# Performance work log

Measured on AMD Instinct MI355X. Metric: run time of the kernel, lower is better.

Reference implementation:

```python
import jax, jax.numpy as jnp
import numpy as np

SMOOTH = 1.0
P = 2
NUM_ITERS = 200  # kornia connected_components num_iterations


def _maxpool3x3(x):
    # F.max_pool2d(x, kernel_size=3, stride=1, padding=1) equivalent (NCHW)
    return jax.lax.reduce_window(
        x, -jnp.inf, jax.lax.max,
        window_dimensions=(1, 1, 3, 3),
        window_strides=(1, 1, 1, 1),
        padding='SAME',
    )


def connected_components(mask_f, num_iterations=NUM_ITERS):
    # kornia-style iterative label propagation on a (B,1,H,W) binary mask.
    # labels initialized to unique pixel ids where mask==1, 0 elsewhere,
    # then 3x3 max-pool propagated, keeping background pinned at 0.
    B, C, H, W = mask_f.shape
    mask = mask_f > 0
    init = jnp.arange(B * C * H * W, dtype=mask_f.dtype).reshape(B, C, H, W)
    out = jnp.where(mask, init, 0.0)

    def body(i, o):
        return jnp.where(mask, _maxpool3x3(o), 0.0)

    return jax.lax.fori_loop(0, num_iterations, body, out)


def setup_inputs() -> dict:
    key = jax.random.key(0)
    k1, k2 = jax.random.split(key)
    B, H, W = 16, 512, 512
    predict = jax.random.uniform(k1, (B, 1, H, W), dtype=jnp.float32)
    target = jax.random.uniform(k2, (B, 1, H, W), dtype=jnp.float32)
    return {"predict": predict, "target": target}


def reference(predict, target):
    B = predict.shape[0]
    # threshold at half of global max -> binary mask (non-differentiable)
    binmask = (predict > (predict.max() / 2)).astype(predict.dtype)
    labels = connected_components(jax.lax.stop_gradient(binmask))

    # torch.numel(torch.unique(labels)) via sort + adjacent-diff count (jit-safe)
    s = jnp.sort(labels.reshape(-1))
    n_unique = 1 + jnp.sum(s[1:] != s[:-1])

    penalty = n_unique.astype(jnp.float32) / B
    penalty = jnp.where(penalty < 1.0, jnp.float32(B), penalty)
    penalty = jnp.minimum(penalty, jnp.float32(B))

    p = predict.reshape(B, -1)
    t = target.reshape(B, -1)
    num = jnp.sum(p * t, axis=1) + SMOOTH
    den = jnp.sum(p ** P + t ** P, axis=1) + SMOOTH
    loss = 1.0 - num / den
    return loss.mean() * penalty  # reduction='mean'
```

## Files before the change

kernel.cpp:

```cpp
#include <hip/hip_runtime.h>
#include <hip/hip_cooperative_groups.h>
#include <stdint.h>

namespace cg = cooperative_groups;

#define NPIX   (16 * 512 * 512)
#define IMG    (512 * 512)
#define NB     16

#define CORE   64
#define HALO   8
#define KIT    8
#define NROUND 25
#define TILE   80
#define TW     88
#define TH     82
#define TX0    4

#define BM_WORDS  (NPIX / 32)
#define NREP      16
#define SAT       256u
#define MAX3(a, b, c) max(max((a), (b)), (c))

__global__ __launch_bounds__(256) void k_max(const float4* __restrict__ p, unsigned int* umax) {
    unsigned int m = 0;
    int base = blockIdx.x * 1024;
#pragma unroll
    for (int k = 0; k < 4; ++k) {
        float4 v = p[base + k * 256 + threadIdx.x];
        m = max(m, __float_as_uint(v.x));
        m = max(m, __float_as_uint(v.y));
        m = max(m, __float_as_uint(v.z));
        m = max(m, __float_as_uint(v.w));
    }
    for (int o = 32; o > 0; o >>= 1)
        m = max(m, (unsigned int)__shfl_down(m, o, 64));
    __shared__ unsigned int sm[4];
    int lane = threadIdx.x & 63, w = threadIdx.x >> 6;
    if (lane == 0) sm[w] = m;
    __syncthreads();
    if (threadIdx.x == 0)
        atomicMax(umax, max(max(sm[0], sm[1]), max(sm[2], sm[3])));
}

__global__ __launch_bounds__(256) void k_init(const float4* __restrict__ pr4,
                                              const float4* __restrict__ tg4,
                                              const unsigned int* __restrict__ umax,
                                              int4* __restrict__ lab4,
                                              float* __restrict__ num, float* __restrict__ den) {
    const float thr = __uint_as_float(*umax) * 0.5f;
    float sn = 0.f, sd = 0.f;
    int base = blockIdx.x * 1024;
#pragma unroll
    for (int k = 0; k < 4; ++k) {
        int i4 = base + k * 256 + threadIdx.x;
        float4 p = pr4[i4], t = tg4[i4];
        int pix = i4 * 4;
        int4 L;
        L.x = (p.x > thr) ? pix     : -1;
        L.y = (p.y > thr) ? pix + 1 : -1;
        L.z = (p.z > thr) ? pix + 2 : -1;
        L.w = (p.w > thr) ? pix + 3 : -1;
        lab4[i4] = L;
        sn += p.x * t.x + p.y * t.y + p.z * t.z + p.w * t.w;
        sd += p.x * p.x + p.y * p.y + p.z * p.z + p.w * p.w
            + t.x * t.x + t.y * t.y + t.z * t.z + t.w * t.w;
    }
    for (int o = 32; o > 0; o >>= 1) {
        sn += __shfl_down(sn, o, 64);
        sd += __shfl_down(sd, o, 64);
    }
    __shared__ float wn[4], wd[4];
    int lane = threadIdx.x & 63, w = threadIdx.x >> 6;
    if (lane == 0) { wn[w] = sn; wd[w] = sd; }
    __syncthreads();
    if (threadIdx.x == 0) {
        int b = blockIdx.x >> 6;
        atomicAdd(&num[b * 32], wn[0] + wn[1] + wn[2] + wn[3]);
        atomicAdd(&den[b * 32], wd[0] + wd[1] + wd[2] + wd[3]);
    }
}

__global__ __launch_bounds__(256) void k_iso(const int* __restrict__ lab,
                                             unsigned int* __restrict__ isoCnt) {
    unsigned int cnt = 0;
    const int tid = threadIdx.x;
    for (int k = 0; k < 8; ++k) {
        int i4 = (blockIdx.x * 8 + k) * 256 + tid;
        int px = i4 * 4;
        int y = (px >> 9) & 511;
        int gxr = px & 511;
        int4 c = *(const int4*)(lab + px);
        int lc = (gxr > 0)   ? lab[px - 1] : -1;
        int rc = (gxr < 508) ? lab[px + 4] : -1;
        int4 u; int lu, ru;
        if (y > 0) {
            u  = *(const int4*)(lab + px - 512);
            lu = (gxr > 0)   ? lab[px - 513] : -1;
            ru = (gxr < 508) ? lab[px - 508] : -1;
        } else { u = make_int4(-1, -1, -1, -1); lu = -1; ru = -1; }
        int4 d; int ld, rd;
        if (y < 511) {
            d  = *(const int4*)(lab + px + 512);
            ld = (gxr > 0)   ? lab[px + 511] : -1;
            rd = (gxr < 508) ? lab[px + 516] : -1;
        } else { d = make_int4(-1, -1, -1, -1); ld = -1; rd = -1; }
        int v0 = max(u.x, d.x), v1 = max(u.y, d.y), v2 = max(u.z, d.z), v3 = max(u.w, d.w);
        int cmL = MAX3(lu, lc, ld), cmR = MAX3(ru, rc, rd);
        int cm0 = max(v0, c.x), cm1 = max(v1, c.y), cm2 = max(v2, c.z), cm3 = max(v3, c.w);
        int nb0 = MAX3(cmL, cm1, v0);
        int nb1 = MAX3(cm0, cm2, v1);
        int nb2 = MAX3(cm1, cm3, v2);
        int nb3 = MAX3(cm2, cmR, v3);
        cnt += (c.x >= 0 && nb0 < 0 && px > 0) ? 1u : 0u;
        cnt += (c.y >= 0 && nb1 < 0) ? 1u : 0u;
        cnt += (c.z >= 0 && nb2 < 0) ? 1u : 0u;
        cnt += (c.w >= 0 && nb3 < 0) ? 1u : 0u;
    }
    for (int o = 32; o > 0; o >>= 1)
        cnt += __shfl_down(cnt, o, 64);
    __shared__ unsigned int sc[4];
    int lane = tid & 63, w = tid >> 6;
    if (lane == 0) sc[w] = cnt;
    __syncthreads();
    if (tid == 0)
        atomicAdd(isoCnt, sc[0] + sc[1] + sc[2] + sc[3]);
}

__global__ __launch_bounds__(256, 4) void k_prop_all(int* __restrict__ bufA,
                                                     int* __restrict__ bufB,
                                                     const unsigned int* __restrict__ isoCnt) {
    if (*isoCnt >= SAT) return;
    cg::grid_group grid = cg::this_grid();
    __shared__ int T[TH * TW];
    const int tid  = threadIdx.x;
    const int blk  = blockIdx.x;
    const int bx   = blk & 7, by = (blk >> 3) & 7, bimg = blk >> 6;
    const int gx0  = bx * CORE - HALO;
    const int gy0  = by * CORE - HALO;
    int* const base0 = bufA + bimg * IMG;
    int* const base1 = bufB + bimg * IMG;

    if (tid < TW) { T[tid] = -1; T[81 * TW + tid] = -1; }
    if (tid < 80) { T[(tid + 1) * TW + 3] = -1; T[(tid + 1) * TW + 84] = -1; }
    for (int u = tid; u < 1600; u += 256) {
        int r = u / 20, c = (u % 20) * 4;
        int gy = gy0 + r, gx = gx0 + c;
        int4 v = (gy >= 0 && gy < 512 && gx >= 0 && gx < 512)
                 ? *(const int4*)(base0 + (gy << 9) + gx)
                 : make_int4(-1, -1, -1, -1);
        *(int4*)&T[(r + 1) * TW + TX0 + c] = v;
    }
    __syncthreads();
    grid.sync();

    const bool active = (tid < 200);
    const int cu = tid % 20, ru = tid / 20;
    const int x0 = cu * 4;
    const int yr = ru * 8;
    int4 O[8];

#define LOAD_ROW(y, V, VL, VR) do {                            \
        const int* _r = &T[((y) + 1) * TW + TX0 + x0];         \
        V  = *(const int4*)_r;                                 \
        VL = _r[-1];                                           \
        VR = _r[4];                                            \
    } while (0)

    for (int r = 0; r < NROUND; ++r) {
        for (int it = 0; it < KIT; ++it) {
            if (active) {
                int4 A, B, C; int Al, Ar, Bl, Br, Cl, Cr;
                LOAD_ROW(yr - 1, A, Al, Ar);
                LOAD_ROW(yr,     B, Bl, Br);
#pragma unroll
                for (int j = 0; j < 8; ++j) {
                    LOAD_ROW(yr + j + 1, C, Cl, Cr);
                    int4 col;
                    col.x = MAX3(A.x, B.x, C.x);
                    col.y = MAX3(A.y, B.y, C.y);
                    col.z = MAX3(A.z, B.z, C.z);
                    col.w = MAX3(A.w, B.w, C.w);
                    int cl = MAX3(Al, Bl, Cl);
                    int cr = MAX3(Ar, Br, Cr);
                    O[j].x = MAX3(cl,    col.x, col.y) | (B.x >> 31);
                    O[j].y = MAX3(col.x, col.y, col.z) | (B.y >> 31);
                    O[j].z = MAX3(col.y, col.z, col.w) | (B.z >> 31);
                    O[j].w = MAX3(col.z, col.w, cr)    | (B.w >> 31);
                    A = B; Al = Bl; Ar = Br;
                    B = C; Bl = Cl; Br = Cr;
                }
            }
            __syncthreads();
            if (active) {
#pragma unroll
                for (int j = 0; j < 8; ++j)
                    *(int4*)&T[(yr + j + 1) * TW + TX0 + x0] = O[j];
            }
            __syncthreads();
        }

        if (r < NROUND - 1) {
            int* dst = (r & 1) ? base1 : base0;
            for (int u = tid; u < 448; u += 256) {
                int lr, lc;
                if (u < 128)      { lr = u >> 4;                lc = u & 15; }
                else if (u < 256) { lr = 56 + ((u - 128) >> 4); lc = u & 15; }
                else { int v = u - 256; lr = 8 + (v >> 2); int s = v & 3; lc = (s < 2) ? s : 12 + s; }
                int4 val = *(const int4*)&T[(HALO + lr + 1) * TW + TX0 + HALO + lc * 4];
                *(int4*)(dst + ((by * CORE + lr) << 9) + bx * CORE + lc * 4) = val;
            }
            __threadfence();
            grid.sync();
            const int* src = (r & 1) ? base1 : base0;
            for (int u = tid; u < 576; u += 256) {
                int lrow, lcu;
                if (u < 160)      { lrow = u / 20;              lcu = u % 20; }
                else if (u < 320) { lrow = 72 + (u - 160) / 20; lcu = u % 20; }
                else { int v = u - 320; lrow = 8 + (v >> 2); int s = v & 3; lcu = (s < 2) ? s : 16 + s; }
                int gy = gy0 + lrow, gx = gx0 + lcu * 4;
                int4 val = (gy >= 0 && gy < 512 && gx >= 0 && gx < 512)
                           ? *(const int4*)(src + (gy << 9) + gx)
                           : make_int4(-1, -1, -1, -1);
                *(int4*)&T[(lrow + 1) * TW + TX0 + lcu * 4] = val;
            }
            __syncthreads();
        } else {
            for (int u = tid; u < 1024; u += 256) {
                int lr = u >> 4, lc = u & 15;
                int4 val = *(const int4*)&T[(HALO + lr + 1) * TW + TX0 + HALO + lc * 4];
                *(int4*)(base0 + ((by * CORE + lr) << 9) + bx * CORE + lc * 4) = val;
            }
        }
    }
#undef LOAD_ROW
}

__global__ __launch_bounds__(256) void k_bits(const int* __restrict__ lab,
                                              unsigned int* __restrict__ bm,
                                              const unsigned int* __restrict__ isoCnt) {
    if (*isoCnt >= SAT) return;
    __shared__ unsigned int sk[1024];
    __shared__ int slot[256];
    const int tid = threadIdx.x;
    unsigned int* rep = bm + (blockIdx.x & (NREP - 1)) * BM_WORDS;
    for (int k = 0; k < 4; ++k) {
        if (k) __syncthreads();
        const int i4 = blockIdx.x * 1024 + k * 256 + tid;
        int4 c = ((const int4*)lab)[i4];
        int pw = __shfl_up(c.w, 1, 64);
        unsigned int prevk;
        if ((tid & 63) == 0) {
            if (i4 == 0) prevk = ~0u;
            else { int pv = lab[i4 * 4 - 1]; prevk = (pv < 0) ? 0u : (unsigned int)pv; }
        } else {
            prevk = (pw < 0) ? 0u : (unsigned int)pw;
        }
        unsigned int k0 = (c.x < 0) ? 0u : (unsigned int)c.x;
        unsigned int k1 = (c.y < 0) ? 0u : (unsigned int)c.y;
        unsigned int k2 = (c.z < 0) ? 0u : (unsigned int)c.z;
        unsigned int k3 = (c.w < 0) ? 0u : (unsigned int)c.w;
        bool c0 = (k0 != prevk), c1 = (k1 != k0), c2 = (k2 != k1), c3 = (k3 != k2);
        sk[0 * 256 + tid] = k0;
        sk[1 * 256 + tid] = k1;
        sk[2 * 256 + tid] = k2;
        sk[3 * 256 + tid] = k3;
        if (c0) slot[k0 & 255] = tid * 4 + 0;
        if (c1) slot[k1 & 255] = tid * 4 + 1;
        if (c2) slot[k2 & 255] = tid * 4 + 2;
        if (c3) slot[k3 & 255] = tid * 4 + 3;
        __syncthreads();
#define SKAT(w) sk[((w) & 3) * 256 + ((w) >> 2)]
        if (c0) { int w = slot[k0 & 255]; if (w != tid * 4 + 0 && SKAT(w) == k0) c0 = false; }
        if (c1) { int w = slot[k1 & 255]; if (w != tid * 4 + 1 && SKAT(w) == k1) c1 = false; }
        if (c2) { int w = slot[k2 & 255]; if (w != tid * 4 + 2 && SKAT(w) == k2) c2 = false; }
        if (c3) { int w = slot[k3 & 255]; if (w != tid * 4 + 3 && SKAT(w) == k3) c3 = false; }
#undef SKAT
#define TSET(kk, cc) if (cc) {                                        \
            unsigned int word = rep[(kk) >> 5];                       \
            if (!((word >> ((kk) & 31)) & 1u))                        \
                atomicOr(&rep[(kk) >> 5], 1u << ((kk) & 31));         \
        }
        TSET(k0, c0); TSET(k1, c1); TSET(k2, c2); TSET(k3, c3);
#undef TSET
    }
}

__global__ void k_popc(const unsigned int* __restrict__ bm, unsigned int* nuniq, int words,
                       const unsigned int* __restrict__ isoCnt) {
    if (*isoCnt >= SAT) return;
    unsigned int c = 0;
    for (int i = blockIdx.x * blockDim.x + threadIdx.x; i < words; i += gridDim.x * blockDim.x) {
        unsigned int w = 0;
#pragma unroll
        for (int r = 0; r < NREP; ++r) w |= bm[r * BM_WORDS + i];
        c += __popc(w);
    }
    for (int o = 32; o > 0; o >>= 1)
        c += __shfl_down(c, o, 64);
    __shared__ unsigned int sc[4];
    int lane = threadIdx.x & 63, w = threadIdx.x >> 6;
    if (lane == 0) sc[w] = c;
    __syncthreads();
    if (threadIdx.x == 0)
        atomicAdd(nuniq, sc[0] + sc[1] + sc[2] + sc[3]);
}

__global__ void k_final(const unsigned int* __restrict__ nuniq,
                        const unsigned int* __restrict__ isoCnt,
                        const float* __restrict__ num, const float* __restrict__ den,
                        float* __restrict__ out) {
    float loss = 0.0f;
    for (int b = 0; b < NB; ++b)
        loss += 1.0f - (num[b * 32] + 1.0f) / (den[b * 32] + 1.0f);
    loss *= (1.0f / NB);
    float penalty;
    if (*isoCnt >= SAT) {
        penalty = (float)NB;
    } else {
        penalty = (float)(*nuniq) / (float)NB;
        if (penalty < 1.0f) penalty = (float)NB;
        penalty = fminf(penalty, (float)NB);
    }
    out[0] = loss * penalty;
}

extern "C" void kernel_launch(void* const* d_in, const int* in_sizes, int n_in,
                              void* d_out, int out_size, void* d_ws, size_t ws_size,
                              hipStream_t stream) {
    const float* predict = (const float*)d_in[0];
    const float* target  = (const float*)d_in[1];
    float* out = (float*)d_out;

    char* ws = (char*)d_ws;
    unsigned int* umax   = (unsigned int*)ws;
    unsigned int* nuniq  = (unsigned int*)(ws + 4);
    unsigned int* isoCnt = (unsigned int*)(ws + 8);
    float* num = (float*)(ws + 256);
    float* den = (float*)(ws + 2304);
    int* labA = (int*)(ws + 16384);
    int* labB = labA + NPIX;
    unsigned int* bm = (unsigned int*)(ws + 16384 + (size_t)2 * NPIX * sizeof(int));

    hipMemsetAsync(ws, 0, 16384, stream);
    hipMemsetAsync(bm, 0, (size_t)NREP * BM_WORDS * sizeof(unsigned int), stream);

    k_max<<<1024, 256, 0, stream>>>((const float4*)predict, umax);
    k_init<<<1024, 256, 0, stream>>>((const float4*)predict, (const float4*)target,
                                     umax, (int4*)labA, num, den);
    k_iso<<<512, 256, 0, stream>>>(labA, isoCnt);

    void* args[] = { (void*)&labA, (void*)&labB, (void*)&isoCnt };
    hipLaunchCooperativeKernel((void*)k_prop_all, dim3(1024), dim3(256), args, 0, stream);

    k_bits<<<NPIX / 4096, 256, 0, stream>>>(labA, bm, isoCnt);
    k_popc<<<512, 256, 0, stream>>>(bm, nuniq, BM_WORDS, isoCnt);
    k_final<<<1, 1, 0, stream>>>(nuniq, isoCnt, num, den, out);
}
```

Measured before the change: 144.2 us.

## Compute isolated-pixel count from predict before init and skip label writes

The isolated-pixel counter now thresholds the predict tensor directly and runs before the init kernel, so init can skip writing the label buffer when the count already saturates. The separate memset of the replicated bitmap is removed and that zeroing is folded into the cooperative propagation kernel. This is meant to remove a full label-buffer write and read plus a memset launch on the saturated path. In exchange, k_iso now does float loads and compares, and the bitmap zeroing happens only when propagation runs. That relies on the downstream kernels also skipping when saturated.

New measurement: 147.2 us. +2.1%, slower.

```diff
diff --git a/kernel.cpp b/kernel.cpp
--- a/kernel.cpp
+++ b/kernel.cpp
@@ -12,7 +12,6 @@
 #define HALO   8
 #define KIT    8
 #define NROUND 25
-#define TILE   80
 #define TW     88
 #define TH     82
 #define TX0    4
@@ -43,79 +42,42 @@
         atomicMax(umax, max(max(sm[0], sm[1]), max(sm[2], sm[3])));
 }
 
-__global__ __launch_bounds__(256) void k_init(const float4* __restrict__ pr4,
-                                              const float4* __restrict__ tg4,
-                                              const unsigned int* __restrict__ umax,
-                                              int4* __restrict__ lab4,
-                                              float* __restrict__ num, float* __restrict__ den) {
+__global__ __launch_bounds__(256) void k_iso(const float* __restrict__ pr,
+                                             const unsigned int* __restrict__ umax,
+                                             unsigned int* __restrict__ isoCnt) {
     const float thr = __uint_as_float(*umax) * 0.5f;
-    float sn = 0.f, sd = 0.f;
-    int base = blockIdx.x * 1024;
-#pragma unroll
-    for (int k = 0; k < 4; ++k) {
-        int i4 = base + k * 256 + threadIdx.x;
-        float4 p = pr4[i4], t = tg4[i4];
-        int pix = i4 * 4;
-        int4 L;
-        L.x = (p.x > thr) ? pix     : -1;
-        L.y = (p.y > thr) ? pix + 1 : -1;
-        L.z = (p.z > thr) ? pix + 2 : -1;
-        L.w = (p.w > thr) ? pix + 3 : -1;
-        lab4[i4] = L;
-        sn += p.x * t.x + p.y * t.y + p.z * t.z + p.w * t.w;
-        sd += p.x * p.x + p.y * p.y + p.z * p.z + p.w * p.w
-            + t.x * t.x + t.y * t.y + t.z * t.z + t.w * t.w;
-    }
-    for (int o = 32; o > 0; o >>= 1) {
-        sn += __shfl_down(sn, o, 64);
-        sd += __shfl_down(sd, o, 64);
-    }
-    __shared__ float wn[4], wd[4];
-    int lane = threadIdx.x & 63, w = threadIdx.x >> 6;
-    if (lane == 0) { wn[w] = sn; wd[w] = sd; }
-    __syncthreads();
-    if (threadIdx.x == 0) {
-        int b = blockIdx.x >> 6;
-        atomicAdd(&num[b * 32], wn[0] + wn[1] + wn[2] + wn[3]);
-        atomicAdd(&den[b * 32], wd[0] + wd[1] + wd[2] + wd[3]);
-    }
-}
-
-__global__ __launch_bounds__(256) void k_iso(const int* __restrict__ lab,
-                                             unsigned int* __restrict__ isoCnt) {
     unsigned int cnt = 0;
     const int tid = threadIdx.x;
     for (int k = 0; k < 8; ++k) {
         int i4 = (blockIdx.x * 8 + k) * 256 + tid;
         int px = i4 * 4;
-        int y = (px >> 9) & 511;
+        int y   = (px >> 9) & 511;
         int gxr = px & 511;
-        int4 c = *(const int4*)(lab + px);
-        int lc = (gxr > 0)   ? lab[px - 1] : -1;
-        int rc = (gxr < 508) ? lab[px + 4] : -1;
-        int4 u; int lu, ru;
+        float4 c = *(const float4*)(pr + px);
+        bool m0 = c.x > thr, m1 = c.y > thr, m2 = c.z > thr, m3 = c.w > thr;
+        bool lc = (gxr > 0)   && pr[px - 1] > thr;
+        bool rc = (gxr < 508) && pr[px + 4] > thr;
+        bool u0 = false, u1 = false, u2 = false, u3 = false, lu = false, ru = false;
         if (y > 0) {
-            u  = *(const int4*)(lab + px - 512);
-            lu = (gxr > 0)   ? lab[px - 513] : -1;
-            ru = (gxr < 508) ? lab[px - 508] : -1;
-        } else { u = make_int4(-1, -1, -1, -1); lu = -1; ru = -1; }
-        int4 d; int ld, rd;
+            float4 u = *(const float4*)(pr + px - 512);
+            u0 = u.x > thr; u1 = u.y > thr; u2 = u.z > thr; u3 = u.w > thr;
+            lu = (gxr > 0)   && pr[px - 513] > thr;
+            ru = (gxr < 508) && pr[px - 508] > thr;
+        }
+        bool d0 = false, d1 = false, d2 = false, d3 = false, ld = false, rd = false;
         if (y < 511) {
-            d  = *(const int4*)(lab + px + 512);
-            ld = (gxr > 0)   ? lab[px + 511] : -1;
-            rd = (gxr < 508) ? lab[px + 516] : -1;
-        } else { d = make_int4(-1, -1, -1, -1); ld = -1; rd = -1; }
-        int v0 = max(u.x, d.x), v1 = max(u.y, d.y), v2 = max(u.z, d.z), v3 = max(u.w, d.w);
-        int cmL = MAX3(lu, lc, ld), cmR = MAX3(ru, rc, rd);
-        int cm0 = max(v0, c.x), cm1 = max(v1, c.y), cm2 = max(v2, c.z), cm3 = max(v3, c.w);
-        int nb0 = MAX3(cmL, cm1, v0);
-        int nb1 = MAX3(cm0, cm2, v1);
-        int nb2 = MAX3(cm1, cm3, v2);
-        int nb3 = MAX3(cm2, cmR, v3);
-        cnt += (c.x >= 0 && nb0 < 0 && px > 0) ? 1u : 0u;
-        cnt += (c.y >= 0 && nb1 < 0) ? 1u : 0u;
-        cnt += (c.z >= 0 && nb2 < 0) ? 1u : 0u;
-        cnt += (c.w >= 0 && nb3 < 0) ? 1u : 0u;
+            float4 d = *(const float4*)(pr + px + 512);
+            d0 = d.x > thr; d1 = d.y > thr; d2 = d.z > thr; d3 = d.w > thr;
+            ld = (gxr > 0)   && pr[px + 511] > thr;
+            rd = (gxr < 508) && pr[px + 516] > thr;
+        }
+        bool v0 = u0 | d0, v1 = u1 | d1, v2 = u2 | d2, v3 = u3 | d3;
+        bool cmL = lu | lc | ld, cmR = ru | rc | rd;
+        bool cm0 = v0 | m0, cm1 = v1 | m1, cm2 = v2 | m2, cm3 = v3 | m3;
+        cnt += (m0 && !(cmL | cm1 | v0) && px > 0) ? 1u : 0u;
+        cnt += (m1 && !(cm0 | cm2 | v1)) ? 1u : 0u;
+        cnt += (m2 && !(cm1 | cm3 | v2)) ? 1u : 0u;
+        cnt += (m3 && !(cm2 | cmR | v3)) ? 1u : 0u;
     }
     for (int o = 32; o > 0; o >>= 1)
         cnt += __shfl_down(cnt, o, 64);
@@ -127,8 +89,51 @@
         atomicAdd(isoCnt, sc[0] + sc[1] + sc[2] + sc[3]);
 }
 
+__global__ __launch_bounds__(256) void k_init(const float4* __restrict__ pr4,
+                                              const float4* __restrict__ tg4,
+                                              const unsigned int* __restrict__ umax,
+                                              const unsigned int* __restrict__ isoCnt,
+                                              int4* __restrict__ lab4,
+                                              float* __restrict__ num, float* __restrict__ den) {
+    const float thr = __uint_as_float(*umax) * 0.5f;
+    const bool wlab = (*isoCnt < SAT);
+    float sn = 0.f, sd = 0.f;
+    int base = blockIdx.x * 1024;
+#pragma unroll
+    for (int k = 0; k < 4; ++k) {
+        int i4 = base + k * 256 + threadIdx.x;
+        float4 p = pr4[i4], t = tg4[i4];
+        if (wlab) {
+            int pix = i4 * 4;
+            int4 L;
+            L.x = (p.x > thr) ? pix     : -1;
+            L.y = (p.y > thr) ? pix + 1 : -1;
+            L.z = (p.z > thr) ? pix + 2 : -1;
+            L.w = (p.w > thr) ? pix + 3 : -1;
+            lab4[i4] = L;
+        }
+        sn += p.x * t.x + p.y * t.y + p.z * t.z + p.w * t.w;
+        sd += p.x * p.x + p.y * p.y + p.z * p.z + p.w * p.w
+            + t.x * t.x + t.y * t.y + t.z * t.z + t.w * t.w;
+    }
+    for (int o = 32; o > 0; o >>= 1) {
+        sn += __shfl_down(sn, o, 64);
+        sd += __shfl_down(sd, o, 64);
+    }
+    __shared__ float wn[4], wd[4];
+    int lane = threadIdx.x & 63, w = threadIdx.x >> 6;
+    if (lane == 0) { wn[w] = sn; wd[w] = sd; }
+    __syncthreads();
+    if (threadIdx.x == 0) {
+        int b = blockIdx.x >> 6;
+        atomicAdd(&num[b * 32], wn[0] + wn[1] + wn[2] + wn[3]);
+        atomicAdd(&den[b * 32], wd[0] + wd[1] + wd[2] + wd[3]);
+    }
+}
+
 __global__ __launch_bounds__(256, 4) void k_prop_all(int* __restrict__ bufA,
                                                      int* __restrict__ bufB,
+                                                     unsigned int* __restrict__ bm,
                                                      const unsigned int* __restrict__ isoCnt) {
     if (*isoCnt >= SAT) return;
     cg::grid_group grid = cg::this_grid();
@@ -140,6 +145,12 @@
     const int gy0  = by * CORE - HALO;
     int* const base0 = bufA + bimg * IMG;
     int* const base1 = bufB + bimg * IMG;
+
+    {
+        int4* bmz = (int4*)bm;
+        for (int u = blk * 256 + tid; u < NREP * BM_WORDS / 4; u += 1024 * 256)
+            bmz[u] = make_int4(0, 0, 0, 0);
+    }
 
     if (tid < TW) { T[tid] = -1; T[81 * TW + tid] = -1; }
     if (tid < 80) { T[(tid + 1) * TW + 3] = -1; T[(tid + 1) * TW + 84] = -1; }
@@ -343,14 +354,13 @@
     unsigned int* bm = (unsigned int*)(ws + 16384 + (size_t)2 * NPIX * sizeof(int));
 
     hipMemsetAsync(ws, 0, 16384, stream);
-    hipMemsetAsync(bm, 0, (size_t)NREP * BM_WORDS * sizeof(unsigned int), stream);
 
     k_max<<<1024, 256, 0, stream>>>((const float4*)predict, umax);
+    k_iso<<<512, 256, 0, stream>>>(predict, umax, isoCnt);
     k_init<<<1024, 256, 0, stream>>>((const float4*)predict, (const float4*)target,
-                                     umax, (int4*)labA, num, den);
-    k_iso<<<512, 256, 0, stream>>>(labA, isoCnt);
-
-    void* args[] = { (void*)&labA, (void*)&labB, (void*)&isoCnt };
+                                     umax, isoCnt, (int4*)labA, num, den);
+
+    void* args[] = { (void*)&labA, (void*)&labB, (void*)&bm, (void*)&isoCnt };
     hipLaunchCooperativeKernel((void*)k_prop_all, dim3(1024), dim3(256), args, 0, stream);
 
     k_bits<<<NPIX / 4096, 256, 0, stream>>>(labA, bm, isoCnt);
```
